# Performance work log

Measured on AMD Instinct MI355X. Metric: run time of the kernel, lower is better.

## Reference

```python
import jax, jax.numpy as jnp
import numpy as np
from jax import lax

DN = ('NCHW', 'OIHW', 'NCHW')

def _dwsep(x, dw, pw_w, pw_b, stride):
    # depthwise: groups = in_channels, kernel (C,1,3,3)
    y = lax.conv_general_dilated(x, dw, (stride, stride), [(1, 1), (1, 1)],
                                 dimension_numbers=DN, feature_group_count=x.shape[1])
    # pointwise 1x1
    y = lax.conv_general_dilated(y, pw_w, (1, 1), 'VALID', dimension_numbers=DN)
    return y + pw_b[None, :, None, None]

def setup_inputs() -> dict:
    key = jax.random.key(0)
    ks = jax.random.split(key, 16)
    s = 0.1
    inp = {
        'flow_raw': jax.random.normal(ks[0], (32, 2, 480, 640), jnp.float32),
        'dw1': jax.random.normal(ks[1], (5, 1, 3, 3), jnp.float32) * s,
        'pw1_w': jax.random.normal(ks[2], (32, 5, 1, 1), jnp.float32) * s,
        'pw1_b': jnp.zeros((32,), jnp.float32),
        'dw2': jax.random.normal(ks[3], (32, 1, 3, 3), jnp.float32) * s,
        'pw2_w': jax.random.normal(ks[4], (64, 32, 1, 1), jnp.float32) * s,
        'pw2_b': jnp.zeros((64,), jnp.float32),
        'dw3': jax.random.normal(ks[5], (64, 1, 3, 3), jnp.float32) * s,
        'pw3_w': jax.random.normal(ks[6], (64, 64, 1, 1), jnp.float32) * s,
        'pw3_b': jnp.zeros((64,), jnp.float32),
        'attn_w': jax.random.normal(ks[7], (1, 64, 1, 1), jnp.float32) * s,
        'attn_b': jnp.zeros((1,), jnp.float32),
        'mlp1_w': jax.random.normal(ks[8], (32, 64), jnp.float32) * s,
        'mlp1_b': jnp.zeros((32,), jnp.float32),
        'mlp2_w': jax.random.normal(ks[9], (3, 32), jnp.float32) * s,
        'mlp2_b': jnp.zeros((3,), jnp.float32),
        'w_ih': jax.random.normal(ks[10], (96, 3), jnp.float32) * s,
        'w_hh': jax.random.normal(ks[11], (96, 32), jnp.float32) * s,
        'b_ih': jnp.zeros((96,), jnp.float32),
        'b_hh': jnp.zeros((96,), jnp.float32),
        'fc_w': jnp.zeros((3, 32), jnp.float32),  # gru_fc init to zero in torch code
        'fc_b': jnp.zeros((3,), jnp.float32),
    }
    return inp

def reference(flow_raw, dw1, pw1_w, pw1_b, dw2, pw2_w, pw2_b, dw3, pw3_w, pw3_b,
              attn_w, attn_b, mlp1_w, mlp1_b, mlp2_w, mlp2_b,
              w_ih, w_hh, b_ih, b_hh, fc_w, fc_b):
    B, _, H, W = flow_raw.shape
    # coordinate channels (x, y, r^2)
    y = jnp.linspace(-1.0, 1.0, H)
    x = jnp.linspace(-1.0, 1.0, W)
    yy, xx = jnp.meshgrid(y, x, indexing='ij')
    coords = jnp.stack([xx, yy, xx**2 + yy**2], axis=0)            # (3,H,W)
    coords_b = jnp.broadcast_to(coords[None], (B, 3, H, W))
    inp = jnp.concatenate([flow_raw, coords_b], axis=1)            # (B,5,H,W)

    f = jax.nn.elu(_dwsep(inp, dw1, pw1_w, pw1_b, 2))              # (B,32,H/2,W/2)
    f = jax.nn.elu(_dwsep(f, dw2, pw2_w, pw2_b, 2))                # (B,64,H/4,W/4)
    f = jax.nn.elu(_dwsep(f, dw3, pw3_w, pw3_b, 2))                # (B,64,H/8,W/8)

    # attention pooling
    logits = jnp.einsum('bchw,oc->bohw', f, attn_w[:, :, 0, 0]) + attn_b[None, :, None, None]
    Bs, _, Hs, Ws = logits.shape
    w = jax.nn.softmax(logits.reshape(Bs, Hs * Ws), axis=-1)       # (B, HW)
    pooled = jnp.einsum('bcn,bn->bc', f.reshape(Bs, 64, Hs * Ws), w)  # (B,64)

    # omega MLP
    h1 = jax.nn.elu(pooled @ mlp1_w.T + mlp1_b)
    omega_inst = h1 @ mlp2_w.T + mlp2_b                            # (B,3)

    # single-step GRU, h0 = 0 (PyTorch gate order: r, z, n)
    h0 = jnp.zeros((B, 32), flow_raw.dtype)
    gi = omega_inst @ w_ih.T + b_ih                                # (B,96)
    gh = h0 @ w_hh.T + b_hh
    i_r, i_z, i_n = jnp.split(gi, 3, axis=-1)
    h_r, h_z, h_n = jnp.split(gh, 3, axis=-1)
    r = jax.nn.sigmoid(i_r + h_r)
    z = jax.nn.sigmoid(i_z + h_z)
    n = jnp.tanh(i_n + r * h_n)
    h = (1.0 - z) * n + z * h0                                     # (B,32)

    delta_omega = h @ fc_w.T + fc_b
    return omega_inst + delta_omega
```

## Files before the change

### kernel.cpp

```cpp
#include <hip/hip_runtime.h>
#include <hip/hip_bf16.h>

#define H0 480
#define W0 640
#define H1 240
#define W1 320
#define H2 120
#define W2 160
#define H3 60
#define W3 80

#define W_PW1T  0
#define W_PW2T  160
#define W_PW3T  2208
#define WBUF_BYTES 65536

#define F2_PB (64 * H2 * W2)
#define F3_PB (64 * H3 * W3)
#define N3    (H3 * W3)

#define TH 8
#define TW 32
#define TILES_W 5
#define TILES_H 15
#define TILES_PB 75
#define F1COLS 65
#define NP 1105
#define LROW 66
#define LCH 1122

typedef float v2f __attribute__((ext_vector_type(2)));

__global__ __launch_bounds__(256) void k_cvt(
    const float* __restrict__ pw1, const float* __restrict__ pw2,
    const float* __restrict__ pw3, float* __restrict__ wb)
{
    int t = threadIdx.x;
    for (int i = t; i < 160;  i += 256) { int o = i / 5,  c = i % 5;  wb[W_PW1T + c*32 + o] = pw1[i]; }
    for (int i = t; i < 2048; i += 256) { int o = i >> 5, c = i & 31; wb[W_PW2T + c*64 + o] = pw2[i]; }
    for (int i = t; i < 4096; i += 256) { int o = i >> 6, c = i & 63; wb[W_PW3T + c*64 + o] = pw3[i]; }
}

template<bool MASK>
__device__ __forceinline__ void fuse12_chunks(
    int t, const float (&dd)[5][5], const float (&vmf)[5], const int (&widx)[5],
    float* __restrict__ f1buf, const float* __restrict__ wb,
    const float* __restrict__ b1, const float* __restrict__ dw2,
    int rbase, v2f (&acc2)[32])
{
    for (int cc = 0; cc < 4; cc++) {
        #pragma unroll
        for (int j = 0; j < 8; j++) {
            int c = cc*8 + j;
            float w10 = wb[W_PW1T + c];
            float w11 = wb[W_PW1T + 32 + c];
            float w12 = wb[W_PW1T + 64 + c];
            float w13 = wb[W_PW1T + 96 + c];
            float w14 = wb[W_PW1T + 128 + c];
            float bc = b1[c];
            #pragma unroll
            for (int i = 0; i < 5; i++) {
                float v = bc;
                v = fmaf(w10, dd[i][0], v);
                v = fmaf(w11, dd[i][1], v);
                v = fmaf(w12, dd[i][2], v);
                v = fmaf(w13, dd[i][3], v);
                v = fmaf(w14, dd[i][4], v);
                float f = v > 0.f ? v : (__expf(v) - 1.f);
                if (MASK) f *= vmf[i];
                if (i < 4)               f1buf[j*LCH + widx[i]] = f;
                else if (t < NP - 1024)  f1buf[j*LCH + widx[4]] = f;
            }
        }
        __syncthreads();
        #pragma unroll
        for (int j = 0; j < 8; j++) {
            int c = cc*8 + j;
            const float* w9 = dw2 + c*9;
            const float* fp = f1buf + j*LCH + rbase;
            float dv = 0.f;
            #pragma unroll
            for (int r = 0; r < 3; r++) {
                dv = fmaf(w9[r*3+0], fp[r*LROW],      dv);
                dv = fmaf(w9[r*3+1], fp[r*LROW + 33], dv);
                dv = fmaf(w9[r*3+2], fp[r*LROW + 1],  dv);
            }
            const v2f* wr2 = (const v2f*)(wb + W_PW2T + c*64);
            v2f dvv = { dv, dv };
            #pragma unroll
            for (int o = 0; o < 32; o++)
                acc2[o] = __builtin_elementwise_fma(wr2[o], dvv, acc2[o]);
        }
        __syncthreads();
    }
}

__global__ __launch_bounds__(256, 3) void k_fuse12(
    const float* __restrict__ flow, const float* __restrict__ dw1,
    const float* __restrict__ b1, const float* __restrict__ dw2,
    const float* __restrict__ b2, const float* __restrict__ wb,
    float* __restrict__ out)
{
    __shared__ float f1buf[8 * LCH];

    const int t = threadIdx.x;
    const int bid = blockIdx.x;
    const int b = bid / TILES_PB;
    const int tile = bid - b * TILES_PB;
    const int oh0 = (tile / TILES_W) * TH;
    const int ow0 = (tile % TILES_W) * TW;

    const float sx = 2.f / (W0 - 1), sy = 2.f / (H0 - 1);

    float cs2[3], rs3[3], cs4[3], rs4[3];
    #pragma unroll
    for (int k = 0; k < 3; k++) {
        cs2[k] = dw1[18+k]   + dw1[21+k]   + dw1[24+k];
        rs3[k] = dw1[27+3*k] + dw1[28+3*k] + dw1[29+3*k];
        cs4[k] = dw1[36+k]   + dw1[39+k]   + dw1[42+k];
        rs4[k] = dw1[36+3*k] + dw1[37+3*k] + dw1[38+3*k];
    }
    const float ax2 = 2.f * sx, ay2 = 2.f * sy;
    float ex[3], fyc[3];
    #pragma unroll
    for (int k = 0; k < 3; k++) { ex[k] = sx*(float)(k-1) - 1.f; fyc[k] = sy*(float)(k-1) - 1.f; }
    const float AX1 = ax2*(cs2[0]+cs2[1]+cs2[2]);
    const float AX0 = cs2[0]*ex[0]+cs2[1]*ex[1]+cs2[2]*ex[2];
    const float AY1 = ay2*(rs3[0]+rs3[1]+rs3[2]);
    const float AY0 = rs3[0]*fyc[0]+rs3[1]*fyc[1]+rs3[2]*fyc[2];
    const float GX2 = ax2*ax2*(cs4[0]+cs4[1]+cs4[2]);
    const float GX1 = 2.f*ax2*(cs4[0]*ex[0]+cs4[1]*ex[1]+cs4[2]*ex[2]);
    const float GX0 = cs4[0]*ex[0]*ex[0]+cs4[1]*ex[1]*ex[1]+cs4[2]*ex[2]*ex[2];
    const float GY2 = ay2*ay2*(rs4[0]+rs4[1]+rs4[2]);
    const float GY1 = 2.f*ay2*(rs4[0]*fyc[0]+rs4[1]*fyc[1]+rs4[2]*fyc[2]);
    const float GY0 = rs4[0]*fyc[0]*fyc[0]+rs4[1]*fyc[1]*fyc[1]+rs4[2]*fyc[2]*fyc[2];

    float dd[5][5];
    float vmf[5];
    int   widx[5];
    const float* fb0 = flow + (size_t)(b*2) * (H0*W0);
    const float* fb1 = fb0 + (size_t)(H0*W0);

    const bool interior = (oh0 > 0) && (ow0 > 0);

    if (interior) {
        #pragma unroll
        for (int i = 0; i < 5; i++) {
            int p = t + i*256; if (p > NP-1) p = NP-1;
            int tr = p / F1COLS;
            int tc = p - tr * F1COLS;
            widx[i] = tr*LROW + (tc & 1)*33 + (tc >> 1);
            vmf[i] = 1.f;
            int fr = 2*oh0 - 1 + tr;
            int fc = 2*ow0 - 1 + tc;
            const float* r0 = fb0 + (size_t)(2*fr - 1) * W0 + (2*fc - 1);
            const float* r1 = fb1 + (size_t)(2*fr - 1) * W0 + (2*fc - 1);
            float a0 = 0.f, a1 = 0.f;
            #pragma unroll
            for (int ky = 0; ky < 3; ky++)
                #pragma unroll
                for (int kx = 0; kx < 3; kx++) {
                    a0 = fmaf(dw1[ky*3+kx],   r0[ky*W0+kx], a0);
                    a1 = fmaf(dw1[9+ky*3+kx], r1[ky*W0+kx], a1);
                }
            dd[i][0] = a0; dd[i][1] = a1;
            float fcf = (float)fc, frf = (float)fr;
            dd[i][2] = fmaf(AX1, fcf, AX0);
            dd[i][3] = fmaf(AY1, frf, AY0);
            dd[i][4] = fmaf(fmaf(GX2, fcf, GX1), fcf, GX0)
                     + fmaf(fmaf(GY2, frf, GY1), frf, GY0);
        }
    } else {
        #pragma unroll
        for (int i = 0; i < 5; i++) {
            int p = t + i*256; if (p > NP-1) p = NP-1;
            int tr = p / F1COLS;
            int tc = p - tr * F1COLS;
            widx[i] = tr*LROW + (tc & 1)*33 + (tc >> 1);
            int fr = 2*oh0 - 1 + tr;
            int fc = 2*ow0 - 1 + tc;
            vmf[i] = (fr >= 0 && fc >= 0) ? 1.f : 0.f;
            if (fr >= 1 && fc >= 1) {
                const float* r0 = fb0 + (size_t)(2*fr - 1) * W0 + (2*fc - 1);
                const float* r1 = fb1 + (size_t)(2*fr - 1) * W0 + (2*fc - 1);
                float a0 = 0.f, a1 = 0.f;
                #pragma unroll
                for (int ky = 0; ky < 3; ky++)
                    #pragma unroll
                    for (int kx = 0; kx < 3; kx++) {
                        a0 = fmaf(dw1[ky*3+kx],   r0[ky*W0+kx], a0);
                        a1 = fmaf(dw1[9+ky*3+kx], r1[ky*W0+kx], a1);
                    }
                dd[i][0] = a0; dd[i][1] = a1;
                float fcf = (float)fc, frf = (float)fr;
                dd[i][2] = fmaf(AX1, fcf, AX0);
                dd[i][3] = fmaf(AY1, frf, AY0);
                dd[i][4] = fmaf(fmaf(GX2, fcf, GX1), fcf, GX0)
                         + fmaf(fmaf(GY2, frf, GY1), frf, GY0);
            } else {
                int frc = fr < 0 ? 0 : fr, fcc = fc < 0 ? 0 : fc;
                int ih0 = 2*frc - 1, iw0 = 2*fcc - 1;
                float mh[3] = { ih0 >= 0 ? 1.f : 0.f, 1.f, 1.f };
                float mw[3] = { iw0 >= 0 ? 1.f : 0.f, 1.f, 1.f };
                int ihx[3] = { ih0 < 0 ? 0 : ih0, ih0 + 1, ih0 + 2 };
                int iwx[3] = { iw0 < 0 ? 0 : iw0, iw0 + 1, iw0 + 2 };
                float a0 = 0.f, a1 = 0.f;
                #pragma unroll
                for (int ky = 0; ky < 3; ky++) {
                    const float* rp0 = fb0 + (size_t)ihx[ky] * W0;
                    const float* rp1 = fb1 + (size_t)ihx[ky] * W0;
                    #pragma unroll
                    for (int kx = 0; kx < 3; kx++) {
                        float m = mh[ky]*mw[kx];
                        a0 = fmaf(dw1[ky*3+kx],   m * rp0[iwx[kx]], a0);
                        a1 = fmaf(dw1[9+ky*3+kx], m * rp1[iwx[kx]], a1);
                    }
                }
                dd[i][0] = a0; dd[i][1] = a1;
                float axv = 0.f, ayv = 0.f, arv = 0.f;
                #pragma unroll
                for (int ky = 0; ky < 3; ky++) {
                    float yv = fmaf((float)(ih0 + ky), sy, -1.f);
                    #pragma unroll
                    for (int kx = 0; kx < 3; kx++) {
                        float xv = fmaf((float)(iw0 + kx), sx, -1.f);
                        float m = mh[ky]*mw[kx];
                        axv = fmaf(dw1[18 + ky*3 + kx], m * xv, axv);
                        ayv = fmaf(dw1[27 + ky*3 + kx], m * yv, ayv);
                        arv = fmaf(dw1[36 + ky*3 + kx], m * (xv*xv + yv*yv), arv);
                    }
                }
                dd[i][2] = axv; dd[i][3] = ayv; dd[i][4] = arv;
            }
        }
    }

    v2f acc2[32];
    #pragma unroll
    for (int o = 0; o < 32; o++) acc2[o] = *(const v2f*)(b2 + 2*o);

    const int lr = t >> 5, lc = t & 31;
    const int rbase = 2*lr*LROW + lc;

    if (interior)
        fuse12_chunks<false>(t, dd, vmf, widx, f1buf, wb, b1, dw2, rbase, acc2);
    else
        fuse12_chunks<true>(t, dd, vmf, widx, f1buf, wb, b1, dw2, rbase, acc2);

    const int oh = oh0 + lr, ow = ow0 + lc;
    size_t obase = ((size_t)b * 64) * (H2*W2) + (size_t)oh * W2 + ow;
    #pragma unroll
    for (int o = 0; o < 32; o++) {
        float va = acc2[o].x, vb2 = acc2[o].y;
        out[obase + (size_t)(2*o)   * (H2*W2)] = va  > 0.f ? va  : (__expf(va)  - 1.f);
        out[obase + (size_t)(2*o+1) * (H2*W2)] = vb2 > 0.f ? vb2 : (__expf(vb2) - 1.f);
    }
}

__global__ __launch_bounds__(256, 4) void k_stage3(
    const float* __restrict__ in, const float* __restrict__ dw3,
    const float* __restrict__ b3, const float* __restrict__ wb,
    const float* __restrict__ attn_w, const float* __restrict__ attn_b,
    float* __restrict__ out, float* __restrict__ lg)
{
    int idx = blockIdx.x * 256 + threadIdx.x;
    int ow = idx % W3; int tmp = idx / W3; int oh = tmp % H3; int b = tmp / H3;
    int ih0 = 2*oh - 1, iw0 = 2*ow - 1;
    float mh[3] = { ih0 >= 0 ? 1.f : 0.f, 1.f, 1.f };
    float mw[3] = { iw0 >= 0 ? 1.f : 0.f, 1.f, 1.f };
    int ihx[3] = { ih0 < 0 ? 0 : ih0, ih0 + 1, ih0 + 2 };
    int iwx[3] = { iw0 < 0 ? 0 : iw0, iw0 + 1, iw0 + 2 };
    float m9[9];
    int off[9];
    #pragma unroll
    for (int ky = 0; ky < 3; ky++)
        #pragma unroll
        for (int kx = 0; kx < 3; kx++) {
            m9[ky*3 + kx] = mh[ky] * mw[kx];
            off[ky*3 + kx] = ihx[ky]*W2 + iwx[kx];
        }

    v2f acc2[32];
    #pragma unroll
    for (int o = 0; o < 32; o++) acc2[o] = *(const v2f*)(b3 + 2*o);

    const float* inb = in + (size_t)b * F2_PB;
    for (int c = 0; c < 64; c++) {
        const float* g = inb + (size_t)c * (H2*W2);
        const float* w9 = dw3 + c*9;
        float dv = 0.f;
        #pragma unroll
        for (int p = 0; p < 9; p++)
            dv = fmaf(w9[p], m9[p] * g[off[p]], dv);
        const v2f* wr2 = (const v2f*)(wb + W_PW3T + c*64);
        v2f dvv = { dv, dv };
        #pragma unroll
        for (int o = 0; o < 32; o++)
            acc2[o] = __builtin_elementwise_fma(wr2[o], dvv, acc2[o]);
    }

    size_t obase = ((size_t)b * 64) * (H3*W3) + (size_t)oh*W3 + ow;
    float logit = attn_b[0];
    #pragma unroll
    for (int o = 0; o < 32; o++) {
        float va = acc2[o].x, vb2 = acc2[o].y;
        float ea = va  > 0.f ? va  : (__expf(va)  - 1.f);
        float eb = vb2 > 0.f ? vb2 : (__expf(vb2) - 1.f);
        out[obase + (size_t)(2*o)  *(H3*W3)] = ea;
        out[obase + (size_t)(2*o+1)*(H3*W3)] = eb;
        logit = fmaf(attn_w[2*o],   ea, logit);
        logit = fmaf(attn_w[2*o+1], eb, logit);
    }
    lg[b*N3 + oh*W3 + ow] = logit;
}

__global__ __launch_bounds__(256) void k_softmax(
    float* __restrict__ lg, float* __restrict__ invs)
{
    int b = blockIdx.x, t = threadIdx.x;
    int lane = t & 63, wid = t >> 6;
    __shared__ float sm[4], ss[4];
    float* base = lg + b*N3;

    float m = -1e30f;
    for (int n = t; n < N3; n += 256) m = fmaxf(m, base[n]);
    #pragma unroll
    for (int o = 32; o; o >>= 1) m = fmaxf(m, __shfl_down(m, o, 64));
    if (lane == 0) sm[wid] = m;
    __syncthreads();
    m = fmaxf(fmaxf(sm[0], sm[1]), fmaxf(sm[2], sm[3]));

    float s = 0.f;
    for (int n = t; n < N3; n += 256) {
        float e = __expf(base[n] - m);
        base[n] = e;
        s += e;
    }
    #pragma unroll
    for (int o = 32; o; o >>= 1) s += __shfl_down(s, o, 64);
    if (lane == 0) ss[wid] = s;
    __syncthreads();
    if (t == 0) invs[b] = 1.f / (ss[0] + ss[1] + ss[2] + ss[3]);
}

__global__ __launch_bounds__(256) void k_pool(
    const float* __restrict__ f3, const float* __restrict__ lg,
    const float* __restrict__ invs, float* __restrict__ pooled)
{
    int bc = blockIdx.x;
    int b = bc >> 6, c = bc & 63;
    int t = threadIdx.x, lane = t & 63, wid = t >> 6;
    __shared__ float sr[4];

    const float4* f = (const float4*)(f3 + (size_t)b * F3_PB + (size_t)c * N3);
    const float4* w = (const float4*)(lg + b*N3);

    float s = 0.f;
    for (int i = t; i < N3/4; i += 256) {
        float4 a = f[i], e = w[i];
        s = fmaf(a.x, e.x, s); s = fmaf(a.y, e.y, s);
        s = fmaf(a.z, e.z, s); s = fmaf(a.w, e.w, s);
    }
    #pragma unroll
    for (int o = 32; o; o >>= 1) s += __shfl_down(s, o, 64);
    if (lane == 0) sr[wid] = s;
    __syncthreads();
    if (t == 0) pooled[bc] = (sr[0] + sr[1] + sr[2] + sr[3]) * invs[b];
}

__global__ __launch_bounds__(64) void k_tail(
    const float* __restrict__ pooled,
    const float* __restrict__ mlp1_w, const float* __restrict__ mlp1_b,
    const float* __restrict__ mlp2_w, const float* __restrict__ mlp2_b,
    const float* __restrict__ w_ih, const float* __restrict__ b_ih,
    const float* __restrict__ b_hh,
    const float* __restrict__ fc_w, const float* __restrict__ fc_b,
    float* __restrict__ out)
{
    __shared__ float s_pooled[64];
    __shared__ float s_h1[32];
    __shared__ float s_om[3];
    __shared__ float s_h[32];
    int t = threadIdx.x, b = blockIdx.x;

    s_pooled[t] = pooled[b*64 + t];
    __syncthreads();

    if (t < 32) {
        float a = mlp1_b[t];
        #pragma unroll 8
        for (int c = 0; c < 64; c++) a = fmaf(mlp1_w[t*64 + c], s_pooled[c], a);
        s_h1[t] = a > 0.f ? a : (__expf(a) - 1.f);
    }
    __syncthreads();
    if (t < 3) {
        float a = mlp2_b[t];
        for (int j = 0; j < 32; j++) a = fmaf(mlp2_w[t*32 + j], s_h1[j], a);
        s_om[t] = a;
    }
    __syncthreads();
    if (t < 32) {
        float gr = b_ih[t], gz = b_ih[32 + t], gn = b_ih[64 + t];
        #pragma unroll
        for (int k = 0; k < 3; k++) {
            float ok = s_om[k];
            gr = fmaf(w_ih[t*3 + k],        ok, gr);
            gz = fmaf(w_ih[(32 + t)*3 + k], ok, gz);
            gn = fmaf(w_ih[(64 + t)*3 + k], ok, gn);
        }
        float hr = b_hh[t], hz = b_hh[32 + t], hn = b_hh[64 + t];
        float r = 1.f / (1.f + __expf(-(gr + hr)));
        float z = 1.f / (1.f + __expf(-(gz + hz)));
        float nn = tanhf(gn + r * hn);
        s_h[t] = (1.f - z) * nn;
    }
    __syncthreads();
    if (t < 3) {
        float dl = fc_b[t];
        for (int j = 0; j < 32; j++) dl = fmaf(fc_w[t*32 + j], s_h[j], dl);
        out[b*3 + t] = s_om[t] + dl;
    }
}

extern "C" void kernel_launch(void* const* d_in, const int* in_sizes, int n_in,
                              void* d_out, int out_size, void* d_ws, size_t ws_size,
                              hipStream_t stream)
{
    const float* flow = (const float*)d_in[0];
    float* wb = (float*)d_ws;

    float* f2     = (float*)((char*)d_ws + WBUF_BYTES);
    float* f3     = f2 + (size_t)32 * F2_PB;
    float* lg     = f3 + (size_t)32 * F3_PB;
    float* invs   = lg + (size_t)32 * N3;
    float* pooled = invs + 32;

    k_cvt<<<1, 256, 0, stream>>>(
        (const float*)d_in[2], (const float*)d_in[5], (const float*)d_in[8], wb);

    k_fuse12<<<32 * TILES_PB, 256, 0, stream>>>(
        flow, (const float*)d_in[1], (const float*)d_in[3],
        (const float*)d_in[4], (const float*)d_in[6], wb, f2);

    k_stage3<<<(32*H3*W3)/256, 256, 0, stream>>>(
        f2, (const float*)d_in[7], (const float*)d_in[9], wb,
        (const float*)d_in[10], (const float*)d_in[11], f3, lg);

    k_softmax<<<32, 256, 0, stream>>>(lg, invs);

    k_pool<<<32*64, 256, 0, stream>>>(f3, lg, invs, pooled);

    k_tail<<<32, 64, 0, stream>>>(pooled,
        (const float*)d_in[12], (const float*)d_in[13],
        (const float*)d_in[14], (const float*)d_in[15],
        (const float*)d_in[16], (const float*)d_in[18],
        (const float*)d_in[19], (const float*)d_in[20],
        (const float*)d_in[21], (float*)d_out);
}
```

Measured before the change: 312.9 us.

## Store stage-2 activations channels-last and vectorize stage-3 depthwise loads

The stage-2 output is now written in NHWC layout with float4 stores of 64 contiguous channels per pixel, instead of 64 strided NCHW stores. Stage 3 reads these with float4 loads per tap and uses a transposed depthwise weight table built in the conversion kernel, then does the pointwise FMAs in chunks of 16 channels. The intent is fewer, wider memory transactions in both kernels. The cost is that adjacent threads in stage 3 now access addresses 256 bytes apart, which can hurt coalescing, and the extra per-chunk registers may add register pressure.

```diff
diff --git a/kernel.cpp b/kernel.cpp
--- a/kernel.cpp
+++ b/kernel.cpp
@@ -13,6 +13,7 @@
 #define W_PW1T  0
 #define W_PW2T  160
 #define W_PW3T  2208
+#define W_DW3T  6304
 #define WBUF_BYTES 65536
 
 #define F2_PB (64 * H2 * W2)
@@ -33,12 +34,14 @@
 
 __global__ __launch_bounds__(256) void k_cvt(
     const float* __restrict__ pw1, const float* __restrict__ pw2,
-    const float* __restrict__ pw3, float* __restrict__ wb)
+    const float* __restrict__ pw3, const float* __restrict__ dw3,
+    float* __restrict__ wb)
 {
     int t = threadIdx.x;
     for (int i = t; i < 160;  i += 256) { int o = i / 5,  c = i % 5;  wb[W_PW1T + c*32 + o] = pw1[i]; }
     for (int i = t; i < 2048; i += 256) { int o = i >> 5, c = i & 31; wb[W_PW2T + c*64 + o] = pw2[i]; }
     for (int i = t; i < 4096; i += 256) { int o = i >> 6, c = i & 63; wb[W_PW3T + c*64 + o] = pw3[i]; }
+    for (int i = t; i < 576;  i += 256) { int p = i >> 6, c = i & 63; wb[W_DW3T + i] = dw3[c*9 + p]; }
 }
 
 template<bool MASK>
@@ -248,18 +251,23 @@
         fuse12_chunks<true>(t, dd, vmf, widx, f1buf, wb, b1, dw2, rbase, acc2);
 
     const int oh = oh0 + lr, ow = ow0 + lc;
-    size_t obase = ((size_t)b * 64) * (H2*W2) + (size_t)oh * W2 + ow;
-    #pragma unroll
-    for (int o = 0; o < 32; o++) {
-        float va = acc2[o].x, vb2 = acc2[o].y;
-        out[obase + (size_t)(2*o)   * (H2*W2)] = va  > 0.f ? va  : (__expf(va)  - 1.f);
-        out[obase + (size_t)(2*o+1) * (H2*W2)] = vb2 > 0.f ? vb2 : (__expf(vb2) - 1.f);
+    float4* op = (float4*)(out + ((size_t)b*(H2*W2) + (size_t)oh*W2 + ow) * 64);
+    #pragma unroll
+    for (int q = 0; q < 16; q++) {
+        float a0 = acc2[2*q].x,   a1 = acc2[2*q].y;
+        float a2 = acc2[2*q+1].x, a3 = acc2[2*q+1].y;
+        float4 v;
+        v.x = a0 > 0.f ? a0 : (__expf(a0) - 1.f);
+        v.y = a1 > 0.f ? a1 : (__expf(a1) - 1.f);
+        v.z = a2 > 0.f ? a2 : (__expf(a2) - 1.f);
+        v.w = a3 > 0.f ? a3 : (__expf(a3) - 1.f);
+        op[q] = v;
     }
 }
 
 __global__ __launch_bounds__(256, 4) void k_stage3(
-    const float* __restrict__ in, const float* __restrict__ dw3,
-    const float* __restrict__ b3, const float* __restrict__ wb,
+    const float* __restrict__ in, const float* __restrict__ b3,
+    const float* __restrict__ wb,
     const float* __restrict__ attn_w, const float* __restrict__ attn_b,
     float* __restrict__ out, float* __restrict__ lg)
 {
@@ -277,7 +285,7 @@
         #pragma unroll
         for (int kx = 0; kx < 3; kx++) {
             m9[ky*3 + kx] = mh[ky] * mw[kx];
-            off[ky*3 + kx] = ihx[ky]*W2 + iwx[kx];
+            off[ky*3 + kx] = (ihx[ky]*W2 + iwx[kx]) * 64;
         }
 
     v2f acc2[32];
@@ -285,18 +293,45 @@
     for (int o = 0; o < 32; o++) acc2[o] = *(const v2f*)(b3 + 2*o);
 
     const float* inb = in + (size_t)b * F2_PB;
-    for (int c = 0; c < 64; c++) {
-        const float* g = inb + (size_t)c * (H2*W2);
-        const float* w9 = dw3 + c*9;
-        float dv = 0.f;
-        #pragma unroll
-        for (int p = 0; p < 9; p++)
-            dv = fmaf(w9[p], m9[p] * g[off[p]], dv);
-        const v2f* wr2 = (const v2f*)(wb + W_PW3T + c*64);
-        v2f dvv = { dv, dv };
-        #pragma unroll
-        for (int o = 0; o < 32; o++)
-            acc2[o] = __builtin_elementwise_fma(wr2[o], dvv, acc2[o]);
+
+    #pragma unroll
+    for (int ck = 0; ck < 4; ck++) {
+        v2f dv2[8];
+        #pragma unroll
+        for (int j = 0; j < 8; j++) dv2[j] = (v2f){0.f, 0.f};
+
+        #pragma unroll
+        for (int p = 0; p < 9; p++) {
+            const float4* tp = (const float4*)(inb + (size_t)off[p] + 16*ck);
+            float4 t0 = tp[0], t1 = tp[1], t2 = tp[2], t3 = tp[3];
+            float mp = m9[p];
+            const v2f* wt = (const v2f*)(wb + W_DW3T + p*64 + 16*ck);
+            v2f tv0 = {t0.x, t0.y}, tv1 = {t0.z, t0.w};
+            v2f tv2 = {t1.x, t1.y}, tv3 = {t1.z, t1.w};
+            v2f tv4 = {t2.x, t2.y}, tv5 = {t2.z, t2.w};
+            v2f tv6 = {t3.x, t3.y}, tv7 = {t3.z, t3.w};
+            dv2[0] = __builtin_elementwise_fma(wt[0]*mp, tv0, dv2[0]);
+            dv2[1] = __builtin_elementwise_fma(wt[1]*mp, tv1, dv2[1]);
+            dv2[2] = __builtin_elementwise_fma(wt[2]*mp, tv2, dv2[2]);
+            dv2[3] = __builtin_elementwise_fma(wt[3]*mp, tv3, dv2[3]);
+            dv2[4] = __builtin_elementwise_fma(wt[4]*mp, tv4, dv2[4]);
+            dv2[5] = __builtin_elementwise_fma(wt[5]*mp, tv5, dv2[5]);
+            dv2[6] = __builtin_elementwise_fma(wt[6]*mp, tv6, dv2[6]);
+            dv2[7] = __builtin_elementwise_fma(wt[7]*mp, tv7, dv2[7]);
+        }
+        #pragma unroll
+        for (int j = 0; j < 8; j++) {
+            int c = 16*ck + 2*j;
+            const v2f* wrA = (const v2f*)(wb + W_PW3T + c*64);
+            const v2f* wrB = (const v2f*)(wb + W_PW3T + (c+1)*64);
+            v2f da = { dv2[j].x, dv2[j].x };
+            v2f db = { dv2[j].y, dv2[j].y };
+            #pragma unroll
+            for (int o = 0; o < 32; o++) {
+                acc2[o] = __builtin_elementwise_fma(wrA[o], da, acc2[o]);
+                acc2[o] = __builtin_elementwise_fma(wrB[o], db, acc2[o]);
+            }
+        }
     }
 
     size_t obase = ((size_t)b * 64) * (H3*W3) + (size_t)oh*W3 + ow;
@@ -436,14 +471,15 @@
     float* pooled = invs + 32;
 
     k_cvt<<<1, 256, 0, stream>>>(
-        (const float*)d_in[2], (const float*)d_in[5], (const float*)d_in[8], wb);
+        (const float*)d_in[2], (const float*)d_in[5], (const float*)d_in[8],
+        (const float*)d_in[7], wb);
 
     k_fuse12<<<32 * TILES_PB, 256, 0, stream>>>(
         flow, (const float*)d_in[1], (const float*)d_in[3],
         (const float*)d_in[4], (const float*)d_in[6], wb, f2);
 
     k_stage3<<<(32*H3*W3)/256, 256, 0, stream>>>(
-        f2, (const float*)d_in[7], (const float*)d_in[9], wb,
+        f2, (const float*)d_in[9], wb,
         (const float*)d_in[10], (const float*)d_in[11], f3, lg);
 
     k_softmax<<<32, 256, 0, stream>>>(lg, invs);
```

Result: slower. 382.4 us (+22.2%).
